# Kernel optimization log

Measured on AMD Instinct MI355X. Metric: run time of the kernel, lower is better.

Reference implementation:

```python
import jax, jax.numpy as jnp
import numpy as np

N_NODES = 50000
N_EDGES = 600000
D = 128
N_GRAPHS = 64


def setup_inputs() -> dict:
    key = jax.random.key(0)
    ks = jax.random.split(key, 16)
    x = jax.random.normal(ks[0], (N_NODES, D), dtype=jnp.float32)
    edge_index = jax.random.randint(ks[1], (2, N_EDGES), 0, N_NODES, dtype=jnp.int64)
    batch = jnp.sort(jax.random.randint(ks[2], (N_NODES,), 0, N_GRAPHS, dtype=jnp.int64))
    s = 1.0 / np.sqrt(D)
    def lin(k, out_d, in_d):
        return jax.random.uniform(k, (out_d, in_d), jnp.float32, -s, s)
    inp = {"x": x, "edge_index": edge_index, "batch": batch}
    for i, base in zip(range(3), (3, 6, 9)):
        inp[f"W_rel{i+1}"] = lin(ks[base], D, D)
        inp[f"b_rel{i+1}"] = jax.random.uniform(ks[base + 1], (D,), jnp.float32, -s, s)
        inp[f"W_root{i+1}"] = lin(ks[base + 2], D, D)
    s5 = 1.0 / np.sqrt(5)
    inp["W1"] = lin(ks[12], 5, D)
    inp["b1"] = jax.random.uniform(ks[13], (5,), jnp.float32, -s, s)
    inp["W2"] = jax.random.uniform(ks[14], (1, 5), jnp.float32, -s5, s5)
    inp["b2"] = jax.random.uniform(ks[15], (1,), jnp.float32, -s5, s5)
    return inp


def graph_conv(x, src, dst, W_rel, b_rel, W_root):
    # PyG GraphConv: out_i = W_root x_i + W_rel * sum_{j->i} x_j + b_rel
    agg = jax.ops.segment_sum(x[src], dst, num_segments=N_NODES)  # [N, D]
    return agg @ W_rel.T + b_rel + x @ W_root.T


def reference(x, edge_index, batch,
              W_rel1, b_rel1, W_root1,
              W_rel2, b_rel2, W_root2,
              W_rel3, b_rel3, W_root3,
              W1, b1, W2, b2):
    src, dst = edge_index[0], edge_index[1]
    h = jax.nn.relu(graph_conv(x, src, dst, W_rel1, b_rel1, W_root1))
    h = jax.nn.relu(graph_conv(h, src, dst, W_rel2, b_rel2, W_root2))
    h = graph_conv(h, src, dst, W_rel3, b_rel3, W_root3)
    # global max pool over graphs
    g = jax.ops.segment_max(h, batch, num_segments=N_GRAPHS)  # [G, D]
    out = jax.nn.relu(g @ W1.T + b1) @ W2.T + b2  # [G, 1]
    return out
```

## Files before the change

kernel.cpp:

```cpp
#include <hip/hip_runtime.h>
#include <float.h>

#define N_NODES 50000
#define N_EDGES 600000
#define D 128
#define N_GRAPHS 64
#define SCAN_T 256
#define SCAN_NBLK ((N_NODES + SCAN_T - 1) / SCAN_T)

typedef __attribute__((ext_vector_type(8))) short short8;
typedef __attribute__((ext_vector_type(4))) float floatx4;

__device__ inline float bf2f(unsigned short h) {
    return __uint_as_float((unsigned)h << 16);
}
__device__ inline unsigned short f2bf(float f) {
    unsigned u = __float_as_uint(f);
    return (unsigned short)((u + 0x7fffu + ((u >> 16) & 1u)) >> 16);
}


__global__ void cast_prep(const float4* __restrict__ x, ushort4* __restrict__ xb, int n4,
                          const float* __restrict__ Wr0, const float* __restrict__ Wo0,
                          const float* __restrict__ Wr1, const float* __restrict__ Wo1,
                          const float* __restrict__ Wr2, const float* __restrict__ Wo2,
                          unsigned short* __restrict__ B0, unsigned short* __restrict__ B1,
                          unsigned short* __restrict__ B2,
                          int* __restrict__ deg, float* __restrict__ g) {
    int idx = blockIdx.x * 256 + threadIdx.x;
    if (idx < N_NODES) deg[idx] = 0;
    if (idx < N_GRAPHS * D) g[idx] = -FLT_MAX;
    if (idx < n4) {
        float4 v = x[idx];
        ushort4 o;
        o.x = f2bf(v.x); o.y = f2bf(v.y); o.z = f2bf(v.z); o.w = f2bf(v.w);
        xb[idx] = o;
        return;
    }
    int w = idx - n4;
    if (w >= 3 * 128 * 256) return;
    int l = w >> 15;
    int r = w & 32767;
    int o = r >> 8, k = r & 255;
    const float* Wr = (l == 0) ? Wr0 : (l == 1) ? Wr1 : Wr2;
    const float* Wo = (l == 0) ? Wo0 : (l == 1) ? Wo1 : Wo2;
    unsigned short* B = (l == 0) ? B0 : (l == 1) ? B1 : B2;
    float v = (k < 128) ? Wr[o * 128 + k] : Wo[o * 128 + (k - 128)];
    B[r] = f2bf(v);
}


__global__ void count_deg(const int* __restrict__ ei, int* __restrict__ deg) {
    int e = blockIdx.x * 256 + threadIdx.x;
    if (e < N_EDGES) atomicAdd(&deg[ei[N_EDGES + e]], 1);
}

__global__ __launch_bounds__(SCAN_T) void block_sum(const int* __restrict__ deg,
                                                    int* __restrict__ blockSums) {
    __shared__ int s[SCAN_T];
    int tid = threadIdx.x;
    int i = blockIdx.x * SCAN_T + tid;
    s[tid] = (i < N_NODES) ? deg[i] : 0;
    __syncthreads();
    for (int off = SCAN_T / 2; off > 0; off >>= 1) {
        if (tid < off) s[tid] += s[tid + off];
        __syncthreads();
    }
    if (tid == 0) blockSums[blockIdx.x] = s[0];
}

__global__ __launch_bounds__(SCAN_T) void scan_write(const int* __restrict__ deg,
                                                     const int* __restrict__ blockSums,
                                                     int* __restrict__ row_start,
                                                     int* __restrict__ cursor) {
    __shared__ int bs[SCAN_T];
    __shared__ int s[SCAN_T];
    int tid = threadIdx.x;
    bs[tid] = (tid < SCAN_NBLK) ? blockSums[tid] : 0;
    __syncthreads();
    for (int off = 1; off < SCAN_T; off <<= 1) {
        int t = (tid >= off) ? bs[tid - off] : 0;
        __syncthreads();
        bs[tid] += t;
        __syncthreads();
    }
    int myOff = (blockIdx.x == 0) ? 0 : bs[blockIdx.x - 1];
    if (blockIdx.x == 0 && tid == SCAN_T - 1) row_start[N_NODES] = bs[tid];

    int i = blockIdx.x * SCAN_T + tid;
    int v = (i < N_NODES) ? deg[i] : 0;
    s[tid] = v;
    __syncthreads();
    for (int off = 1; off < SCAN_T; off <<= 1) {
        int t = (tid >= off) ? s[tid - off] : 0;
        __syncthreads();
        s[tid] += t;
        __syncthreads();
    }
    if (i < N_NODES) {
        int rs = myOff + s[tid] - v;
        row_start[i] = rs;
        cursor[i]    = rs;
    }
}

__global__ void fill_csr(const int* __restrict__ ei, int* __restrict__ cursor,
                         int* __restrict__ csr_src) {
    int e = blockIdx.x * 256 + threadIdx.x;
    if (e < N_EDGES) {
        int dst = ei[N_EDGES + e];
        int pos = atomicAdd(&cursor[dst], 1);
        csr_src[pos] = ei[e];
    }
}


__global__ __launch_bounds__(256) void csr_gather_bf16(
    const unsigned short* __restrict__ xb, const int* __restrict__ row_start,
    const int* __restrict__ csr_src, unsigned short* __restrict__ aggb)
{
    int node = blockIdx.x * 8 + (threadIdx.x >> 5);
    int lane = threadIdx.x & 31;
    if (node >= N_NODES) return;
    int beg = row_start[node];
    int end = row_start[node + 1];

    float a0 = 0.f, a1 = 0.f, a2 = 0.f, a3 = 0.f;
    for (int base = beg; base < end; base += 32) {
        int n = end - base; if (n > 32) n = 32;
        int idx = (lane < n) ? csr_src[base + lane] : 0;
        int j = 0;
        for (; j + 7 < n; j += 8) {
            int s0 = __shfl(idx, j,     32); int s1 = __shfl(idx, j + 1, 32);
            int s2 = __shfl(idx, j + 2, 32); int s3 = __shfl(idx, j + 3, 32);
            int s4 = __shfl(idx, j + 4, 32); int s5 = __shfl(idx, j + 5, 32);
            int s6 = __shfl(idx, j + 6, 32); int s7 = __shfl(idx, j + 7, 32);
            ushort4 u0 = *(const ushort4*)(xb + (size_t)s0 * D + lane * 4);
            ushort4 u1 = *(const ushort4*)(xb + (size_t)s1 * D + lane * 4);
            ushort4 u2 = *(const ushort4*)(xb + (size_t)s2 * D + lane * 4);
            ushort4 u3 = *(const ushort4*)(xb + (size_t)s3 * D + lane * 4);
            ushort4 u4 = *(const ushort4*)(xb + (size_t)s4 * D + lane * 4);
            ushort4 u5 = *(const ushort4*)(xb + (size_t)s5 * D + lane * 4);
            ushort4 u6 = *(const ushort4*)(xb + (size_t)s6 * D + lane * 4);
            ushort4 u7 = *(const ushort4*)(xb + (size_t)s7 * D + lane * 4);
            a0 += bf2f(u0.x) + bf2f(u1.x) + bf2f(u2.x) + bf2f(u3.x)
                + bf2f(u4.x) + bf2f(u5.x) + bf2f(u6.x) + bf2f(u7.x);
            a1 += bf2f(u0.y) + bf2f(u1.y) + bf2f(u2.y) + bf2f(u3.y)
                + bf2f(u4.y) + bf2f(u5.y) + bf2f(u6.y) + bf2f(u7.y);
            a2 += bf2f(u0.z) + bf2f(u1.z) + bf2f(u2.z) + bf2f(u3.z)
                + bf2f(u4.z) + bf2f(u5.z) + bf2f(u6.z) + bf2f(u7.z);
            a3 += bf2f(u0.w) + bf2f(u1.w) + bf2f(u2.w) + bf2f(u3.w)
                + bf2f(u4.w) + bf2f(u5.w) + bf2f(u6.w) + bf2f(u7.w);
        }
        for (; j + 3 < n; j += 4) {
            int s0 = __shfl(idx, j,     32); int s1 = __shfl(idx, j + 1, 32);
            int s2 = __shfl(idx, j + 2, 32); int s3 = __shfl(idx, j + 3, 32);
            ushort4 u0 = *(const ushort4*)(xb + (size_t)s0 * D + lane * 4);
            ushort4 u1 = *(const ushort4*)(xb + (size_t)s1 * D + lane * 4);
            ushort4 u2 = *(const ushort4*)(xb + (size_t)s2 * D + lane * 4);
            ushort4 u3 = *(const ushort4*)(xb + (size_t)s3 * D + lane * 4);
            a0 += bf2f(u0.x) + bf2f(u1.x) + bf2f(u2.x) + bf2f(u3.x);
            a1 += bf2f(u0.y) + bf2f(u1.y) + bf2f(u2.y) + bf2f(u3.y);
            a2 += bf2f(u0.z) + bf2f(u1.z) + bf2f(u2.z) + bf2f(u3.z);
            a3 += bf2f(u0.w) + bf2f(u1.w) + bf2f(u2.w) + bf2f(u3.w);
        }
        for (; j < n; ++j) {
            int s0 = __shfl(idx, j, 32);
            ushort4 u0 = *(const ushort4*)(xb + (size_t)s0 * D + lane * 4);
            a0 += bf2f(u0.x); a1 += bf2f(u0.y); a2 += bf2f(u0.z); a3 += bf2f(u0.w);
        }
    }
    ushort4 r;
    r.x = f2bf(a0); r.y = f2bf(a1); r.z = f2bf(a2); r.w = f2bf(a3);
    *(ushort4*)(aggb + (size_t)node * D + lane * 4) = r;
}


__device__ inline void stage_b_half(unsigned short* sB, const unsigned short* __restrict__ Bb,
                                    int tid, int h) {
#pragma unroll
    for (int i = 0; i < 8; ++i) {
        int flat = tid + i * 256;
        int fi = flat >> 6, ln = flat & 63;
        int mm = ln & 15, qq = ln >> 4;
        int ksL = fi >> 3, tt = fi & 7;
        short8 v = *(const short8*)(Bb + (size_t)(tt * 16 + mm) * 256
                                    + (h * 4 + ksL) * 32 + qq * 8);
        *(short8*)(sB + (size_t)flat * 8) = v;
    }
}


__global__ __launch_bounds__(256) void gemm_mfma(
    const unsigned short* __restrict__ aggb, const unsigned short* __restrict__ xb,
    const unsigned short* __restrict__ Bb, const float* __restrict__ bias,
    unsigned short* __restrict__ Ob, int relu)
{
    __shared__ unsigned short sB[16384];
    int tid  = threadIdx.x;
    int wave = tid >> 6;
    int lane = tid & 63;
    int m    = lane & 15;
    int quad = lane >> 4;
    int row0 = blockIdx.x * 64 + wave * 16;

    int arow = row0 + m;
    if (arow > N_NODES - 1) arow = N_NODES - 1;

    short8 af[8];
#pragma unroll
    for (int ks = 0; ks < 8; ++ks) {
        const unsigned short* Asrc = (ks < 4) ? aggb : xb;
        af[ks] = *(const short8*)(Asrc + (size_t)arow * 128 + (ks & 3) * 32 + quad * 8);
    }

    floatx4 acc[8];
#pragma unroll
    for (int t = 0; t < 8; ++t) acc[t] = (floatx4){0.f, 0.f, 0.f, 0.f};

    stage_b_half(sB, Bb, tid, 0);
    __syncthreads();
#pragma unroll
    for (int ksL = 0; ksL < 4; ++ksL)
#pragma unroll
        for (int t = 0; t < 8; ++t) {
            short8 b = *(const short8*)(sB + (size_t)((ksL * 8 + t) * 64 + lane) * 8);
            acc[t] = __builtin_amdgcn_mfma_f32_16x16x32_bf16(af[ksL], b, acc[t], 0, 0, 0);
        }
    __syncthreads();
    stage_b_half(sB, Bb, tid, 1);
    __syncthreads();
#pragma unroll
    for (int ksL = 0; ksL < 4; ++ksL)
#pragma unroll
        for (int t = 0; t < 8; ++t) {
            short8 b = *(const short8*)(sB + (size_t)((ksL * 8 + t) * 64 + lane) * 8);
            acc[t] = __builtin_amdgcn_mfma_f32_16x16x32_bf16(af[4 + ksL], b, acc[t], 0, 0, 0);
        }

#pragma unroll
    for (int t = 0; t < 8; ++t) {
        int col = t * 16 + m;
        float bv = bias[col];
#pragma unroll
        for (int r = 0; r < 4; ++r) {
            int row = row0 + quad * 4 + r;
            if (row >= N_NODES) continue;
            float v = acc[t][r] + bv;
            if (relu) v = fmaxf(v, 0.f);
            Ob[(size_t)row * D + col] = f2bf(v);
        }
    }
}


struct PoolShared {
    union {
        unsigned short b[16384];
        float c[64 * 129];
    };
};

__global__ __launch_bounds__(256) void gemm_pool(
    const unsigned short* __restrict__ aggb, const unsigned short* __restrict__ xb,
    const unsigned short* __restrict__ Bb, const float* __restrict__ bias,
    const int* __restrict__ batch, float* __restrict__ g)
{
    __shared__ PoolShared sh;
    __shared__ int bl[64];
    int tid  = threadIdx.x;
    int wave = tid >> 6;
    int lane = tid & 63;
    int m    = lane & 15;
    int quad = lane >> 4;
    int row0 = blockIdx.x * 64;

    int arow = row0 + wave * 16 + m;
    if (arow > N_NODES - 1) arow = N_NODES - 1;

    short8 af[8];
#pragma unroll
    for (int ks = 0; ks < 8; ++ks) {
        const unsigned short* Asrc = (ks < 4) ? aggb : xb;
        af[ks] = *(const short8*)(Asrc + (size_t)arow * 128 + (ks & 3) * 32 + quad * 8);
    }

    floatx4 acc[8];
#pragma unroll
    for (int t = 0; t < 8; ++t) acc[t] = (floatx4){0.f, 0.f, 0.f, 0.f};

    stage_b_half(sh.b, Bb, tid, 0);
    __syncthreads();
#pragma unroll
    for (int ksL = 0; ksL < 4; ++ksL)
#pragma unroll
        for (int t = 0; t < 8; ++t) {
            short8 b = *(const short8*)(sh.b + (size_t)((ksL * 8 + t) * 64 + lane) * 8);
            acc[t] = __builtin_amdgcn_mfma_f32_16x16x32_bf16(af[ksL], b, acc[t], 0, 0, 0);
        }
    __syncthreads();
    stage_b_half(sh.b, Bb, tid, 1);
    __syncthreads();
#pragma unroll
    for (int ksL = 0; ksL < 4; ++ksL)
#pragma unroll
        for (int t = 0; t < 8; ++t) {
            short8 b = *(const short8*)(sh.b + (size_t)((ksL * 8 + t) * 64 + lane) * 8);
            acc[t] = __builtin_amdgcn_mfma_f32_16x16x32_bf16(af[4 + ksL], b, acc[t], 0, 0, 0);
        }
    __syncthreads();

#pragma unroll
    for (int t = 0; t < 8; ++t) {
        int col = t * 16 + m;
        float bv = bias[col];
#pragma unroll
        for (int r = 0; r < 4; ++r)
            sh.c[(wave * 16 + quad * 4 + r) * 129 + col] = acc[t][r] + bv;
    }
    if (tid < 64) {
        int grow = row0 + tid;
        bl[tid] = (grow < N_NODES) ? batch[grow] : -1;
    }
    __syncthreads();

    int nvalid = min(64, N_NODES - row0);
    int b0 = bl[0], b1 = bl[nvalid - 1];
    int col  = tid & 127;
    int rbeg = (tid >> 7) * 32;
    for (int gg = b0; gg <= b1; ++gg) {
        float cur = -FLT_MAX;
#pragma unroll
        for (int r = 0; r < 32; ++r) {
            int rr = rbeg + r;
            float v = (bl[rr] == gg) ? sh.c[rr * 129 + col] : -FLT_MAX;
            cur = fmaxf(cur, v);
        }
        if (cur > -FLT_MAX) {
            float* ad = &g[gg * D + col];
            if (cur >= 0.f) atomicMax((int*)ad, __float_as_int(cur));
            else            atomicMin((unsigned int*)ad, __float_as_uint(cur));
        }
    }
}


__global__ void mlp_head(const float* __restrict__ g,
                         const float* __restrict__ W1, const float* __restrict__ b1,
                         const float* __restrict__ W2, const float* __restrict__ b2,
                         float* __restrict__ out) {
    int gi = threadIdx.x;
    if (gi >= N_GRAPHS) return;
    float h[5];
#pragma unroll
    for (int j = 0; j < 5; ++j) {
        float acc = b1[j];
        for (int k = 0; k < D; ++k) acc += g[gi * D + k] * W1[j * D + k];
        h[j] = fmaxf(acc, 0.f);
    }
    float o = b2[0];
#pragma unroll
    for (int j = 0; j < 5; ++j) o += h[j] * W2[j];
    out[gi] = o;
}

extern "C" void kernel_launch(void* const* d_in, const int* in_sizes, int n_in,
                              void* d_out, int out_size, void* d_ws, size_t ws_size,
                              hipStream_t stream) {
    const float* x     = (const float*)d_in[0];
    const int*   ei    = (const int*)d_in[1];
    const int*   batch = (const int*)d_in[2];
    const float* Wrel[3]  = {(const float*)d_in[3], (const float*)d_in[6], (const float*)d_in[9]};
    const float* brel[3]  = {(const float*)d_in[4], (const float*)d_in[7], (const float*)d_in[10]};
    const float* Wroot[3] = {(const float*)d_in[5], (const float*)d_in[8], (const float*)d_in[11]};
    const float* W1 = (const float*)d_in[12];
    const float* b1 = (const float*)d_in[13];
    const float* W2 = (const float*)d_in[14];
    const float* b2 = (const float*)d_in[15];
    float* out = (float*)d_out;

    char* ws = (char*)d_ws;
    const size_t nodeB16 = (size_t)N_NODES * D * sizeof(unsigned short);
    unsigned short* xb   = (unsigned short*)(ws);
    unsigned short* aggb = (unsigned short*)(ws + nodeB16);
    unsigned short* hb1  = (unsigned short*)(ws + 2 * nodeB16);
    unsigned short* hb2  = (unsigned short*)(ws + 3 * nodeB16);
    char* p = ws + 4 * nodeB16;
    unsigned short* Bb0 = (unsigned short*)p;   p += 128 * 256 * sizeof(unsigned short);
    unsigned short* Bb1 = (unsigned short*)p;   p += 128 * 256 * sizeof(unsigned short);
    unsigned short* Bb2 = (unsigned short*)p;   p += 128 * 256 * sizeof(unsigned short);
    float* g        = (float*)p;                p += N_GRAPHS * D * sizeof(float);
    int*   deg      = (int*)p;                  p += N_NODES * sizeof(int);
    int*   row_start= (int*)p;                  p += (N_NODES + 1) * sizeof(int);
    int*   cursor   = (int*)p;                  p += N_NODES * sizeof(int);
    int*   csr_src  = (int*)p;                  p += N_EDGES * sizeof(int);
    int*   blockSums= (int*)p;                  p += SCAN_NBLK * sizeof(int);

    const int n4 = N_NODES * D / 4;
    const int cast_total = n4 + 3 * 128 * 256;
    cast_prep<<<(cast_total + 255) / 256, 256, 0, stream>>>(
        (const float4*)x, (ushort4*)xb, n4,
        Wrel[0], Wroot[0], Wrel[1], Wroot[1], Wrel[2], Wroot[2],
        Bb0, Bb1, Bb2, deg, g);

    count_deg<<<(N_EDGES + 255) / 256, 256, 0, stream>>>(ei, deg);
    block_sum<<<SCAN_NBLK, SCAN_T, 0, stream>>>(deg, blockSums);
    scan_write<<<SCAN_NBLK, SCAN_T, 0, stream>>>(deg, blockSums, row_start, cursor);
    fill_csr<<<(N_EDGES + 255) / 256, 256, 0, stream>>>(ei, cursor, csr_src);

    const int ggrid = (N_NODES + 7) / 8;
    const int mgrid = (N_NODES + 63) / 64;

    csr_gather_bf16<<<ggrid, 256, 0, stream>>>(xb, row_start, csr_src, aggb);
    gemm_mfma<<<mgrid, 256, 0, stream>>>(aggb, xb, Bb0, brel[0], hb1, 1);

    csr_gather_bf16<<<ggrid, 256, 0, stream>>>(hb1, row_start, csr_src, aggb);
    gemm_mfma<<<mgrid, 256, 0, stream>>>(aggb, hb1, Bb1, brel[1], hb2, 1);

    csr_gather_bf16<<<ggrid, 256, 0, stream>>>(hb2, row_start, csr_src, aggb);
    gemm_pool<<<mgrid, 256, 0, stream>>>(aggb, hb2, Bb2, brel[2], batch, g);

    mlp_head<<<1, 64, 0, stream>>>(g, W1, b1, W2, b2, out);
}
```

Measured before the change: 309.8 us.

## Fuse CSR neighbor gather into MFMA GEMM kernels via swizzled LDS tile

After: 327.2 us. 5.6% more time.

```diff
diff --git a/kernel.cpp b/kernel.cpp
--- a/kernel.cpp
+++ b/kernel.cpp
@@ -115,64 +115,70 @@
 }
 
 
-__global__ __launch_bounds__(256) void csr_gather_bf16(
-    const unsigned short* __restrict__ xb, const int* __restrict__ row_start,
-    const int* __restrict__ csr_src, unsigned short* __restrict__ aggb)
+#define ACC8(u) { a[0] += bf2f((unsigned short)(u)[0]); a[1] += bf2f((unsigned short)(u)[1]); \
+                  a[2] += bf2f((unsigned short)(u)[2]); a[3] += bf2f((unsigned short)(u)[3]); \
+                  a[4] += bf2f((unsigned short)(u)[4]); a[5] += bf2f((unsigned short)(u)[5]); \
+                  a[6] += bf2f((unsigned short)(u)[6]); a[7] += bf2f((unsigned short)(u)[7]); }
+
+__device__ inline void gather_tile(const unsigned short* __restrict__ xb,
+                                   const int* __restrict__ row_start,
+                                   const int* __restrict__ csr_src,
+                                   unsigned short* sA, int row0, int tid)
 {
-    int node = blockIdx.x * 8 + (threadIdx.x >> 5);
-    int lane = threadIdx.x & 31;
-    if (node >= N_NODES) return;
-    int beg = row_start[node];
-    int end = row_start[node + 1];
-
-    float a0 = 0.f, a1 = 0.f, a2 = 0.f, a3 = 0.f;
-    for (int base = beg; base < end; base += 32) {
-        int n = end - base; if (n > 32) n = 32;
-        int idx = (lane < n) ? csr_src[base + lane] : 0;
-        int j = 0;
-        for (; j + 7 < n; j += 8) {
-            int s0 = __shfl(idx, j,     32); int s1 = __shfl(idx, j + 1, 32);
-            int s2 = __shfl(idx, j + 2, 32); int s3 = __shfl(idx, j + 3, 32);
-            int s4 = __shfl(idx, j + 4, 32); int s5 = __shfl(idx, j + 5, 32);
-            int s6 = __shfl(idx, j + 6, 32); int s7 = __shfl(idx, j + 7, 32);
-            ushort4 u0 = *(const ushort4*)(xb + (size_t)s0 * D + lane * 4);
-            ushort4 u1 = *(const ushort4*)(xb + (size_t)s1 * D + lane * 4);
-            ushort4 u2 = *(const ushort4*)(xb + (size_t)s2 * D + lane * 4);
-            ushort4 u3 = *(const ushort4*)(xb + (size_t)s3 * D + lane * 4);
-            ushort4 u4 = *(const ushort4*)(xb + (size_t)s4 * D + lane * 4);
-            ushort4 u5 = *(const ushort4*)(xb + (size_t)s5 * D + lane * 4);
-            ushort4 u6 = *(const ushort4*)(xb + (size_t)s6 * D + lane * 4);
-            ushort4 u7 = *(const ushort4*)(xb + (size_t)s7 * D + lane * 4);
-            a0 += bf2f(u0.x) + bf2f(u1.x) + bf2f(u2.x) + bf2f(u3.x)
-                + bf2f(u4.x) + bf2f(u5.x) + bf2f(u6.x) + bf2f(u7.x);
-            a1 += bf2f(u0.y) + bf2f(u1.y) + bf2f(u2.y) + bf2f(u3.y)
-                + bf2f(u4.y) + bf2f(u5.y) + bf2f(u6.y) + bf2f(u7.y);
-            a2 += bf2f(u0.z) + bf2f(u1.z) + bf2f(u2.z) + bf2f(u3.z)
-                + bf2f(u4.z) + bf2f(u5.z) + bf2f(u6.z) + bf2f(u7.z);
-            a3 += bf2f(u0.w) + bf2f(u1.w) + bf2f(u2.w) + bf2f(u3.w)
-                + bf2f(u4.w) + bf2f(u5.w) + bf2f(u6.w) + bf2f(u7.w);
-        }
-        for (; j + 3 < n; j += 4) {
-            int s0 = __shfl(idx, j,     32); int s1 = __shfl(idx, j + 1, 32);
-            int s2 = __shfl(idx, j + 2, 32); int s3 = __shfl(idx, j + 3, 32);
-            ushort4 u0 = *(const ushort4*)(xb + (size_t)s0 * D + lane * 4);
-            ushort4 u1 = *(const ushort4*)(xb + (size_t)s1 * D + lane * 4);
-            ushort4 u2 = *(const ushort4*)(xb + (size_t)s2 * D + lane * 4);
-            ushort4 u3 = *(const ushort4*)(xb + (size_t)s3 * D + lane * 4);
-            a0 += bf2f(u0.x) + bf2f(u1.x) + bf2f(u2.x) + bf2f(u3.x);
-            a1 += bf2f(u0.y) + bf2f(u1.y) + bf2f(u2.y) + bf2f(u3.y);
-            a2 += bf2f(u0.z) + bf2f(u1.z) + bf2f(u2.z) + bf2f(u3.z);
-            a3 += bf2f(u0.w) + bf2f(u1.w) + bf2f(u2.w) + bf2f(u3.w);
-        }
-        for (; j < n; ++j) {
-            int s0 = __shfl(idx, j, 32);
-            ushort4 u0 = *(const ushort4*)(xb + (size_t)s0 * D + lane * 4);
-            a0 += bf2f(u0.x); a1 += bf2f(u0.y); a2 += bf2f(u0.z); a3 += bf2f(u0.w);
-        }
-    }
-    ushort4 r;
-    r.x = f2bf(a0); r.y = f2bf(a1); r.z = f2bf(a2); r.w = f2bf(a3);
-    *(ushort4*)(aggb + (size_t)node * D + lane * 4) = r;
+    int grp = tid >> 4;
+    int ln  = tid & 15;
+#pragma unroll 1
+    for (int pass = 0; pass < 4; ++pass) {
+        int r = pass * 16 + grp;
+        int node = row0 + r;
+        float a[8];
+#pragma unroll
+        for (int i = 0; i < 8; ++i) a[i] = 0.f;
+        if (node < N_NODES) {
+            int beg = row_start[node];
+            int end = row_start[node + 1];
+            for (int base = beg; base < end; base += 16) {
+                int n = end - base; if (n > 16) n = 16;
+                int idx = (ln < n) ? csr_src[base + ln] : 0;
+                int j = 0;
+                for (; j + 7 < n; j += 8) {
+                    int s0 = __shfl(idx, j,     16); int s1 = __shfl(idx, j + 1, 16);
+                    int s2 = __shfl(idx, j + 2, 16); int s3 = __shfl(idx, j + 3, 16);
+                    int s4 = __shfl(idx, j + 4, 16); int s5 = __shfl(idx, j + 5, 16);
+                    int s6 = __shfl(idx, j + 6, 16); int s7 = __shfl(idx, j + 7, 16);
+                    short8 u0 = *(const short8*)(xb + (size_t)s0 * D + ln * 8);
+                    short8 u1 = *(const short8*)(xb + (size_t)s1 * D + ln * 8);
+                    short8 u2 = *(const short8*)(xb + (size_t)s2 * D + ln * 8);
+                    short8 u3 = *(const short8*)(xb + (size_t)s3 * D + ln * 8);
+                    short8 u4 = *(const short8*)(xb + (size_t)s4 * D + ln * 8);
+                    short8 u5 = *(const short8*)(xb + (size_t)s5 * D + ln * 8);
+                    short8 u6 = *(const short8*)(xb + (size_t)s6 * D + ln * 8);
+                    short8 u7 = *(const short8*)(xb + (size_t)s7 * D + ln * 8);
+                    ACC8(u0); ACC8(u1); ACC8(u2); ACC8(u3);
+                    ACC8(u4); ACC8(u5); ACC8(u6); ACC8(u7);
+                }
+                for (; j + 3 < n; j += 4) {
+                    int s0 = __shfl(idx, j,     16); int s1 = __shfl(idx, j + 1, 16);
+                    int s2 = __shfl(idx, j + 2, 16); int s3 = __shfl(idx, j + 3, 16);
+                    short8 u0 = *(const short8*)(xb + (size_t)s0 * D + ln * 8);
+                    short8 u1 = *(const short8*)(xb + (size_t)s1 * D + ln * 8);
+                    short8 u2 = *(const short8*)(xb + (size_t)s2 * D + ln * 8);
+                    short8 u3 = *(const short8*)(xb + (size_t)s3 * D + ln * 8);
+                    ACC8(u0); ACC8(u1); ACC8(u2); ACC8(u3);
+                }
+                for (; j < n; ++j) {
+                    int s0 = __shfl(idx, j, 16);
+                    short8 u0 = *(const short8*)(xb + (size_t)s0 * D + ln * 8);
+                    ACC8(u0);
+                }
+            }
+        }
+        short8 v;
+#pragma unroll
+        for (int i = 0; i < 8; ++i) v[i] = (short)f2bf(a[i]);
+        int slot = r * 16 + (ln ^ (r & 7));
+        *(short8*)((char*)sA + (size_t)slot * 16) = v;
+    }
 }
 
 
@@ -191,41 +197,53 @@
 }
 
 
-__global__ __launch_bounds__(256) void gemm_mfma(
-    const unsigned short* __restrict__ aggb, const unsigned short* __restrict__ xb,
-    const unsigned short* __restrict__ Bb, const float* __restrict__ bias,
-    unsigned short* __restrict__ Ob, int relu)
+__global__ __launch_bounds__(256) void layer_fused(
+    const unsigned short* __restrict__ xb, const int* __restrict__ row_start,
+    const int* __restrict__ csr_src, const unsigned short* __restrict__ Bb,
+    const float* __restrict__ bias, unsigned short* __restrict__ Ob, int relu)
 {
+    __shared__ unsigned short sA[64 * 128];
     __shared__ unsigned short sB[16384];
     int tid  = threadIdx.x;
+    int row0 = blockIdx.x * 64;
+
+    gather_tile(xb, row_start, csr_src, sA, row0, tid);
+
     int wave = tid >> 6;
     int lane = tid & 63;
     int m    = lane & 15;
     int quad = lane >> 4;
-    int row0 = blockIdx.x * 64 + wave * 16;
-
-    int arow = row0 + m;
+
+    int arow = row0 + wave * 16 + m;
     if (arow > N_NODES - 1) arow = N_NODES - 1;
-
-    short8 af[8];
-#pragma unroll
-    for (int ks = 0; ks < 8; ++ks) {
-        const unsigned short* Asrc = (ks < 4) ? aggb : xb;
-        af[ks] = *(const short8*)(Asrc + (size_t)arow * 128 + (ks & 3) * 32 + quad * 8);
+    short8 afX[4];
+#pragma unroll
+    for (int ks = 0; ks < 4; ++ks)
+        afX[ks] = *(const short8*)(xb + (size_t)arow * 128 + ks * 32 + quad * 8);
+
+    stage_b_half(sB, Bb, tid, 0);
+    __syncthreads();
+
+    short8 afA[4];
+    {
+        int r = wave * 16 + m;
+#pragma unroll
+        for (int ksL = 0; ksL < 4; ++ksL) {
+            int slot = r * 16 + ((ksL * 4 + quad) ^ (r & 7));
+            afA[ksL] = *(const short8*)((const char*)sA + (size_t)slot * 16);
+        }
     }
 
     floatx4 acc[8];
 #pragma unroll
     for (int t = 0; t < 8; ++t) acc[t] = (floatx4){0.f, 0.f, 0.f, 0.f};
 
-    stage_b_half(sB, Bb, tid, 0);
-    __syncthreads();
 #pragma unroll
     for (int ksL = 0; ksL < 4; ++ksL)
 #pragma unroll
         for (int t = 0; t < 8; ++t) {
             short8 b = *(const short8*)(sB + (size_t)((ksL * 8 + t) * 64 + lane) * 8);
-            acc[t] = __builtin_amdgcn_mfma_f32_16x16x32_bf16(af[ksL], b, acc[t], 0, 0, 0);
+            acc[t] = __builtin_amdgcn_mfma_f32_16x16x32_bf16(afA[ksL], b, acc[t], 0, 0, 0);
         }
     __syncthreads();
     stage_b_half(sB, Bb, tid, 1);
@@ -235,7 +253,7 @@
 #pragma unroll
         for (int t = 0; t < 8; ++t) {
             short8 b = *(const short8*)(sB + (size_t)((ksL * 8 + t) * 64 + lane) * 8);
-            acc[t] = __builtin_amdgcn_mfma_f32_16x16x32_bf16(af[4 + ksL], b, acc[t], 0, 0, 0);
+            acc[t] = __builtin_amdgcn_mfma_f32_16x16x32_bf16(afX[ksL], b, acc[t], 0, 0, 0);
         }
 
 #pragma unroll
@@ -244,7 +262,7 @@
         float bv = bias[col];
 #pragma unroll
         for (int r = 0; r < 4; ++r) {
-            int row = row0 + quad * 4 + r;
+            int row = row0 + wave * 16 + quad * 4 + r;
             if (row >= N_NODES) continue;
             float v = acc[t][r] + bv;
             if (relu) v = fmaxf(v, 0.f);
@@ -261,42 +279,58 @@
     };
 };
 
-__global__ __launch_bounds__(256) void gemm_pool(
-    const unsigned short* __restrict__ aggb, const unsigned short* __restrict__ xb,
-    const unsigned short* __restrict__ Bb, const float* __restrict__ bias,
-    const int* __restrict__ batch, float* __restrict__ g)
+__global__ __launch_bounds__(256) void layer_pool(
+    const unsigned short* __restrict__ xb, const int* __restrict__ row_start,
+    const int* __restrict__ csr_src, const unsigned short* __restrict__ Bb,
+    const float* __restrict__ bias, const int* __restrict__ batch, float* __restrict__ g)
 {
+    __shared__ unsigned short sA[64 * 128];
     __shared__ PoolShared sh;
     __shared__ int bl[64];
     int tid  = threadIdx.x;
+    int row0 = blockIdx.x * 64;
+
+    gather_tile(xb, row_start, csr_src, sA, row0, tid);
+
     int wave = tid >> 6;
     int lane = tid & 63;
     int m    = lane & 15;
     int quad = lane >> 4;
-    int row0 = blockIdx.x * 64;
 
     int arow = row0 + wave * 16 + m;
     if (arow > N_NODES - 1) arow = N_NODES - 1;
-
-    short8 af[8];
-#pragma unroll
-    for (int ks = 0; ks < 8; ++ks) {
-        const unsigned short* Asrc = (ks < 4) ? aggb : xb;
-        af[ks] = *(const short8*)(Asrc + (size_t)arow * 128 + (ks & 3) * 32 + quad * 8);
+    short8 afX[4];
+#pragma unroll
+    for (int ks = 0; ks < 4; ++ks)
+        afX[ks] = *(const short8*)(xb + (size_t)arow * 128 + ks * 32 + quad * 8);
+
+    if (tid < 64) {
+        int grow = row0 + tid;
+        bl[tid] = (grow < N_NODES) ? batch[grow] : -1;
+    }
+    stage_b_half(sh.b, Bb, tid, 0);
+    __syncthreads();
+
+    short8 afA[4];
+    {
+        int r = wave * 16 + m;
+#pragma unroll
+        for (int ksL = 0; ksL < 4; ++ksL) {
+            int slot = r * 16 + ((ksL * 4 + quad) ^ (r & 7));
+            afA[ksL] = *(const short8*)((const char*)sA + (size_t)slot * 16);
+        }
     }
 
     floatx4 acc[8];
 #pragma unroll
     for (int t = 0; t < 8; ++t) acc[t] = (floatx4){0.f, 0.f, 0.f, 0.f};
 
-    stage_b_half(sh.b, Bb, tid, 0);
-    __syncthreads();
 #pragma unroll
     for (int ksL = 0; ksL < 4; ++ksL)
 #pragma unroll
         for (int t = 0; t < 8; ++t) {
             short8 b = *(const short8*)(sh.b + (size_t)((ksL * 8 + t) * 64 + lane) * 8);
-            acc[t] = __builtin_amdgcn_mfma_f32_16x16x32_bf16(af[ksL], b, acc[t], 0, 0, 0);
+            acc[t] = __builtin_amdgcn_mfma_f32_16x16x32_bf16(afA[ksL], b, acc[t], 0, 0, 0);
         }
     __syncthreads();
     stage_b_half(sh.b, Bb, tid, 1);
@@ -306,7 +340,7 @@
 #pragma unroll
         for (int t = 0; t < 8; ++t) {
             short8 b = *(const short8*)(sh.b + (size_t)((ksL * 8 + t) * 64 + lane) * 8);
-            acc[t] = __builtin_amdgcn_mfma_f32_16x16x32_bf16(af[4 + ksL], b, acc[t], 0, 0, 0);
+            acc[t] = __builtin_amdgcn_mfma_f32_16x16x32_bf16(afX[ksL], b, acc[t], 0, 0, 0);
         }
     __syncthreads();
 
@@ -317,10 +351,6 @@
 #pragma unroll
         for (int r = 0; r < 4; ++r)
             sh.c[(wave * 16 + quad * 4 + r) * 129 + col] = acc[t][r] + bv;
-    }
-    if (tid < 64) {
-        int grow = row0 + tid;
-        bl[tid] = (grow < N_NODES) ? batch[grow] : -1;
     }
     __syncthreads();
 
@@ -345,23 +375,23 @@
 }
 
 
-__global__ void mlp_head(const float* __restrict__ g,
+__global__ __launch_bounds__(64) void mlp_head(const float* __restrict__ g,
                          const float* __restrict__ W1, const float* __restrict__ b1,
                          const float* __restrict__ W2, const float* __restrict__ b2,
                          float* __restrict__ out) {
-    int gi = threadIdx.x;
-    if (gi >= N_GRAPHS) return;
-    float h[5];
+    int gi = blockIdx.x;
+    int lane = threadIdx.x;
+    float x0 = g[gi * D + lane];
+    float x1 = g[gi * D + 64 + lane];
+    float o = b2[0];
 #pragma unroll
     for (int j = 0; j < 5; ++j) {
-        float acc = b1[j];
-        for (int k = 0; k < D; ++k) acc += g[gi * D + k] * W1[j * D + k];
-        h[j] = fmaxf(acc, 0.f);
-    }
-    float o = b2[0];
-#pragma unroll
-    for (int j = 0; j < 5; ++j) o += h[j] * W2[j];
-    out[gi] = o;
+        float p = x0 * W1[j * D + lane] + x1 * W1[j * D + 64 + lane];
+#pragma unroll
+        for (int off = 32; off > 0; off >>= 1) p += __shfl_xor(p, off, 64);
+        o += fmaxf(p + b1[j], 0.f) * W2[j];
+    }
+    if (lane == 0) out[gi] = o;
 }
 
 extern "C" void kernel_launch(void* const* d_in, const int* in_sizes, int n_in,
@@ -382,10 +412,9 @@
     char* ws = (char*)d_ws;
     const size_t nodeB16 = (size_t)N_NODES * D * sizeof(unsigned short);
     unsigned short* xb   = (unsigned short*)(ws);
-    unsigned short* aggb = (unsigned short*)(ws + nodeB16);
-    unsigned short* hb1  = (unsigned short*)(ws + 2 * nodeB16);
-    unsigned short* hb2  = (unsigned short*)(ws + 3 * nodeB16);
-    char* p = ws + 4 * nodeB16;
+    unsigned short* hb1  = (unsigned short*)(ws + nodeB16);
+    unsigned short* hb2  = (unsigned short*)(ws + 2 * nodeB16);
+    char* p = ws + 3 * nodeB16;
     unsigned short* Bb0 = (unsigned short*)p;   p += 128 * 256 * sizeof(unsigned short);
     unsigned short* Bb1 = (unsigned short*)p;   p += 128 * 256 * sizeof(unsigned short);
     unsigned short* Bb2 = (unsigned short*)p;   p += 128 * 256 * sizeof(unsigned short);
@@ -408,17 +437,11 @@
     scan_write<<<SCAN_NBLK, SCAN_T, 0, stream>>>(deg, blockSums, row_start, cursor);
     fill_csr<<<(N_EDGES + 255) / 256, 256, 0, stream>>>(ei, cursor, csr_src);
 
-    const int ggrid = (N_NODES + 7) / 8;
     const int mgrid = (N_NODES + 63) / 64;
 
-    csr_gather_bf16<<<ggrid, 256, 0, stream>>>(xb, row_start, csr_src, aggb);
-    gemm_mfma<<<mgrid, 256, 0, stream>>>(aggb, xb, Bb0, brel[0], hb1, 1);
-
-    csr_gather_bf16<<<ggrid, 256, 0, stream>>>(hb1, row_start, csr_src, aggb);
-    gemm_mfma<<<mgrid, 256, 0, stream>>>(aggb, hb1, Bb1, brel[1], hb2, 1);
-
-    csr_gather_bf16<<<ggrid, 256, 0, stream>>>(hb2, row_start, csr_src, aggb);
-    gemm_pool<<<mgrid, 256, 0, stream>>>(aggb, hb2, Bb2, brel[2], batch, g);
-
-    mlp_head<<<1, 64, 0, stream>>>(g, W1, b1, W2, b2, out);
-}
+    layer_fused<<<mgrid, 256, 0, stream>>>(xb,  row_start, csr_src, Bb0, brel[0], hb1, 1);
+    layer_fused<<<mgrid, 256, 0, stream>>>(hb1, row_start, csr_src, Bb1, brel[1], hb2, 1);
+    layer_pool <<<mgrid, 256, 0, stream>>>(hb2, row_start, csr_src, Bb2, brel[2], batch, g);
+
+    mlp_head<<<N_GRAPHS, 64, 0, stream>>>(g, W1, b1, W2, b2, out);
+}
```

## Split node features into two 64-column halves and gather each half separately

Applied to the files above, without the earlier changes.

Measured after the change: 321.8 us. 3.9% more time.

```diff
diff --git a/kernel.cpp b/kernel.cpp
--- a/kernel.cpp
+++ b/kernel.cpp
@@ -20,7 +20,8 @@
 }
 
 
-__global__ void cast_prep(const float4* __restrict__ x, ushort4* __restrict__ xb, int n4,
+__global__ void cast_prep(const float4* __restrict__ x,
+                          ushort4* __restrict__ xb0, ushort4* __restrict__ xb1, int n4,
                           const float* __restrict__ Wr0, const float* __restrict__ Wo0,
                           const float* __restrict__ Wr1, const float* __restrict__ Wo1,
                           const float* __restrict__ Wr2, const float* __restrict__ Wo2,
@@ -34,7 +35,10 @@
         float4 v = x[idx];
         ushort4 o;
         o.x = f2bf(v.x); o.y = f2bf(v.y); o.z = f2bf(v.z); o.w = f2bf(v.w);
-        xb[idx] = o;
+        int node = idx >> 5;
+        int q    = idx & 31;
+        ushort4* dst = (q < 16) ? xb0 : xb1;
+        dst[(size_t)node * 16 + (q & 15)] = o;
         return;
     }
     int w = idx - n4;
@@ -115,64 +119,66 @@
 }
 
 
-__global__ __launch_bounds__(256) void csr_gather_bf16(
-    const unsigned short* __restrict__ xb, const int* __restrict__ row_start,
-    const int* __restrict__ csr_src, unsigned short* __restrict__ aggb)
+#define ACC8(u) { a[0] += bf2f((unsigned short)(u)[0]); a[1] += bf2f((unsigned short)(u)[1]); \
+                  a[2] += bf2f((unsigned short)(u)[2]); a[3] += bf2f((unsigned short)(u)[3]); \
+                  a[4] += bf2f((unsigned short)(u)[4]); a[5] += bf2f((unsigned short)(u)[5]); \
+                  a[6] += bf2f((unsigned short)(u)[6]); a[7] += bf2f((unsigned short)(u)[7]); }
+
+__global__ __launch_bounds__(256) void gather_half(
+    const unsigned short* __restrict__ xh,
+    const int* __restrict__ row_start, const int* __restrict__ csr_src,
+    unsigned short* __restrict__ aggh)
 {
-    int node = blockIdx.x * 8 + (threadIdx.x >> 5);
-    int lane = threadIdx.x & 31;
+    int grp  = threadIdx.x >> 3;
+    int ln   = threadIdx.x & 7;
+    int node = blockIdx.x * 32 + grp;
     if (node >= N_NODES) return;
     int beg = row_start[node];
     int end = row_start[node + 1];
 
-    float a0 = 0.f, a1 = 0.f, a2 = 0.f, a3 = 0.f;
-    for (int base = beg; base < end; base += 32) {
-        int n = end - base; if (n > 32) n = 32;
-        int idx = (lane < n) ? csr_src[base + lane] : 0;
+    float a[8];
+#pragma unroll
+    for (int i = 0; i < 8; ++i) a[i] = 0.f;
+
+    for (int base = beg; base < end; base += 8) {
+        int n = end - base; if (n > 8) n = 8;
+        int idx = (ln < n) ? csr_src[base + ln] : 0;
         int j = 0;
         for (; j + 7 < n; j += 8) {
-            int s0 = __shfl(idx, j,     32); int s1 = __shfl(idx, j + 1, 32);
-            int s2 = __shfl(idx, j + 2, 32); int s3 = __shfl(idx, j + 3, 32);
-            int s4 = __shfl(idx, j + 4, 32); int s5 = __shfl(idx, j + 5, 32);
-            int s6 = __shfl(idx, j + 6, 32); int s7 = __shfl(idx, j + 7, 32);
-            ushort4 u0 = *(const ushort4*)(xb + (size_t)s0 * D + lane * 4);
-            ushort4 u1 = *(const ushort4*)(xb + (size_t)s1 * D + lane * 4);
-            ushort4 u2 = *(const ushort4*)(xb + (size_t)s2 * D + lane * 4);
-            ushort4 u3 = *(const ushort4*)(xb + (size_t)s3 * D + lane * 4);
-            ushort4 u4 = *(const ushort4*)(xb + (size_t)s4 * D + lane * 4);
-            ushort4 u5 = *(const ushort4*)(xb + (size_t)s5 * D + lane * 4);
-            ushort4 u6 = *(const ushort4*)(xb + (size_t)s6 * D + lane * 4);
-            ushort4 u7 = *(const ushort4*)(xb + (size_t)s7 * D + lane * 4);
-            a0 += bf2f(u0.x) + bf2f(u1.x) + bf2f(u2.x) + bf2f(u3.x)
-                + bf2f(u4.x) + bf2f(u5.x) + bf2f(u6.x) + bf2f(u7.x);
-            a1 += bf2f(u0.y) + bf2f(u1.y) + bf2f(u2.y) + bf2f(u3.y)
-                + bf2f(u4.y) + bf2f(u5.y) + bf2f(u6.y) + bf2f(u7.y);
-            a2 += bf2f(u0.z) + bf2f(u1.z) + bf2f(u2.z) + bf2f(u3.z)
-                + bf2f(u4.z) + bf2f(u5.z) + bf2f(u6.z) + bf2f(u7.z);
-            a3 += bf2f(u0.w) + bf2f(u1.w) + bf2f(u2.w) + bf2f(u3.w)
-                + bf2f(u4.w) + bf2f(u5.w) + bf2f(u6.w) + bf2f(u7.w);
+            int s0 = __shfl(idx, 0, 8); int s1 = __shfl(idx, 1, 8);
+            int s2 = __shfl(idx, 2, 8); int s3 = __shfl(idx, 3, 8);
+            int s4 = __shfl(idx, 4, 8); int s5 = __shfl(idx, 5, 8);
+            int s6 = __shfl(idx, 6, 8); int s7 = __shfl(idx, 7, 8);
+            short8 u0 = *(const short8*)(xh + (size_t)s0 * 64 + ln * 8);
+            short8 u1 = *(const short8*)(xh + (size_t)s1 * 64 + ln * 8);
+            short8 u2 = *(const short8*)(xh + (size_t)s2 * 64 + ln * 8);
+            short8 u3 = *(const short8*)(xh + (size_t)s3 * 64 + ln * 8);
+            short8 u4 = *(const short8*)(xh + (size_t)s4 * 64 + ln * 8);
+            short8 u5 = *(const short8*)(xh + (size_t)s5 * 64 + ln * 8);
+            short8 u6 = *(const short8*)(xh + (size_t)s6 * 64 + ln * 8);
+            short8 u7 = *(const short8*)(xh + (size_t)s7 * 64 + ln * 8);
+            ACC8(u0); ACC8(u1); ACC8(u2); ACC8(u3);
+            ACC8(u4); ACC8(u5); ACC8(u6); ACC8(u7);
         }
         for (; j + 3 < n; j += 4) {
-            int s0 = __shfl(idx, j,     32); int s1 = __shfl(idx, j + 1, 32);
-            int s2 = __shfl(idx, j + 2, 32); int s3 = __shfl(idx, j + 3, 32);
-            ushort4 u0 = *(const ushort4*)(xb + (size_t)s0 * D + lane * 4);
-            ushort4 u1 = *(const ushort4*)(xb + (size_t)s1 * D + lane * 4);
-            ushort4 u2 = *(const ushort4*)(xb + (size_t)s2 * D + lane * 4);
-            ushort4 u3 = *(const ushort4*)(xb + (size_t)s3 * D + lane * 4);
-            a0 += bf2f(u0.x) + bf2f(u1.x) + bf2f(u2.x) + bf2f(u3.x);
-            a1 += bf2f(u0.y) + bf2f(u1.y) + bf2f(u2.y) + bf2f(u3.y);
-            a2 += bf2f(u0.z) + bf2f(u1.z) + bf2f(u2.z) + bf2f(u3.z);
-            a3 += bf2f(u0.w) + bf2f(u1.w) + bf2f(u2.w) + bf2f(u3.w);
+            int s0 = __shfl(idx, j,     8); int s1 = __shfl(idx, j + 1, 8);
+            int s2 = __shfl(idx, j + 2, 8); int s3 = __shfl(idx, j + 3, 8);
+            short8 u0 = *(const short8*)(xh + (size_t)s0 * 64 + ln * 8);
+            short8 u1 = *(const short8*)(xh + (size_t)s1 * 64 + ln * 8);
+            short8 u2 = *(const short8*)(xh + (size_t)s2 * 64 + ln * 8);
+            short8 u3 = *(const short8*)(xh + (size_t)s3 * 64 + ln * 8);
+            ACC8(u0); ACC8(u1); ACC8(u2); ACC8(u3);
         }
         for (; j < n; ++j) {
-            int s0 = __shfl(idx, j, 32);
-            ushort4 u0 = *(const ushort4*)(xb + (size_t)s0 * D + lane * 4);
-            a0 += bf2f(u0.x); a1 += bf2f(u0.y); a2 += bf2f(u0.z); a3 += bf2f(u0.w);
-        }
-    }
-    ushort4 r;
-    r.x = f2bf(a0); r.y = f2bf(a1); r.z = f2bf(a2); r.w = f2bf(a3);
-    *(ushort4*)(aggb + (size_t)node * D + lane * 4) = r;
+            int s0 = __shfl(idx, j, 8);
+            short8 u0 = *(const short8*)(xh + (size_t)s0 * 64 + ln * 8);
+            ACC8(u0);
+        }
+    }
+    short8 r;
+#pragma unroll
+    for (int i = 0; i < 8; ++i) r[i] = (short)f2bf(a[i]);
+    *(short8*)(aggh + (size_t)node * 64 + ln * 8) = r;
 }
 
 
@@ -192,9 +198,10 @@
 
 
 __global__ __launch_bounds__(256) void gemm_mfma(
-    const unsigned short* __restrict__ aggb, const unsigned short* __restrict__ xb,
+    const unsigned short* __restrict__ agg0, const unsigned short* __restrict__ agg1,
+    const unsigned short* __restrict__ x0,   const unsigned short* __restrict__ x1,
     const unsigned short* __restrict__ Bb, const float* __restrict__ bias,
-    unsigned short* __restrict__ Ob, int relu)
+    unsigned short* __restrict__ O0, unsigned short* __restrict__ O1, int relu)
 {
     __shared__ unsigned short sB[16384];
     int tid  = threadIdx.x;
@@ -210,8 +217,9 @@
     short8 af[8];
 #pragma unroll
     for (int ks = 0; ks < 8; ++ks) {
-        const unsigned short* Asrc = (ks < 4) ? aggb : xb;
-        af[ks] = *(const short8*)(Asrc + (size_t)arow * 128 + (ks & 3) * 32 + quad * 8);
+        const unsigned short* Asrc =
+            (ks < 2) ? agg0 : (ks < 4) ? agg1 : (ks < 6) ? x0 : x1;
+        af[ks] = *(const short8*)(Asrc + (size_t)arow * 64 + (ks & 1) * 32 + quad * 8);
     }
 
     floatx4 acc[8];
@@ -242,13 +250,14 @@
     for (int t = 0; t < 8; ++t) {
         int col = t * 16 + m;
         float bv = bias[col];
+        unsigned short* Oh = (t < 4) ? O0 : O1;
 #pragma unroll
         for (int r = 0; r < 4; ++r) {
             int row = row0 + quad * 4 + r;
             if (row >= N_NODES) continue;
             float v = acc[t][r] + bv;
             if (relu) v = fmaxf(v, 0.f);
-            Ob[(size_t)row * D + col] = f2bf(v);
+            Oh[(size_t)row * 64 + (col & 63)] = f2bf(v);
         }
     }
 }
@@ -262,7 +271,8 @@
 };
 
 __global__ __launch_bounds__(256) void gemm_pool(
-    const unsigned short* __restrict__ aggb, const unsigned short* __restrict__ xb,
+    const unsigned short* __restrict__ agg0, const unsigned short* __restrict__ agg1,
+    const unsigned short* __restrict__ x0,   const unsigned short* __restrict__ x1,
     const unsigned short* __restrict__ Bb, const float* __restrict__ bias,
     const int* __restrict__ batch, float* __restrict__ g)
 {
@@ -281,14 +291,19 @@
     short8 af[8];
 #pragma unroll
     for (int ks = 0; ks < 8; ++ks) {
-        const unsigned short* Asrc = (ks < 4) ? aggb : xb;
-        af[ks] = *(const short8*)(Asrc + (size_t)arow * 128 + (ks & 3) * 32 + quad * 8);
+        const unsigned short* Asrc =
+            (ks < 2) ? agg0 : (ks < 4) ? agg1 : (ks < 6) ? x0 : x1;
+        af[ks] = *(const short8*)(Asrc + (size_t)arow * 64 + (ks & 1) * 32 + quad * 8);
     }
 
     floatx4 acc[8];
 #pragma unroll
     for (int t = 0; t < 8; ++t) acc[t] = (floatx4){0.f, 0.f, 0.f, 0.f};
 
+    if (tid < 64) {
+        int grow = row0 + tid;
+        bl[tid] = (grow < N_NODES) ? batch[grow] : -1;
+    }
     stage_b_half(sh.b, Bb, tid, 0);
     __syncthreads();
 #pragma unroll
@@ -317,10 +332,6 @@
 #pragma unroll
         for (int r = 0; r < 4; ++r)
             sh.c[(wave * 16 + quad * 4 + r) * 129 + col] = acc[t][r] + bv;
-    }
-    if (tid < 64) {
-        int grow = row0 + tid;
-        bl[tid] = (grow < N_NODES) ? batch[grow] : -1;
     }
     __syncthreads();
 
@@ -345,23 +356,23 @@
 }
 
 
-__global__ void mlp_head(const float* __restrict__ g,
+__global__ __launch_bounds__(64) void mlp_head(const float* __restrict__ g,
                          const float* __restrict__ W1, const float* __restrict__ b1,
                          const float* __restrict__ W2, const float* __restrict__ b2,
                          float* __restrict__ out) {
-    int gi = threadIdx.x;
-    if (gi >= N_GRAPHS) return;
-    float h[5];
+    int gi = blockIdx.x;
+    int lane = threadIdx.x;
+    float x0 = g[gi * D + lane];
+    float x1 = g[gi * D + 64 + lane];
+    float o = b2[0];
 #pragma unroll
     for (int j = 0; j < 5; ++j) {
-        float acc = b1[j];
-        for (int k = 0; k < D; ++k) acc += g[gi * D + k] * W1[j * D + k];
-        h[j] = fmaxf(acc, 0.f);
-    }
-    float o = b2[0];
-#pragma unroll
-    for (int j = 0; j < 5; ++j) o += h[j] * W2[j];
-    out[gi] = o;
+        float p = x0 * W1[j * D + lane] + x1 * W1[j * D + 64 + lane];
+#pragma unroll
+        for (int off = 32; off > 0; off >>= 1) p += __shfl_xor(p, off, 64);
+        o += fmaxf(p + b1[j], 0.f) * W2[j];
+    }
+    if (lane == 0) out[gi] = o;
 }
 
 extern "C" void kernel_launch(void* const* d_in, const int* in_sizes, int n_in,
@@ -380,12 +391,16 @@
     float* out = (float*)d_out;
 
     char* ws = (char*)d_ws;
-    const size_t nodeB16 = (size_t)N_NODES * D * sizeof(unsigned short);
-    unsigned short* xb   = (unsigned short*)(ws);
-    unsigned short* aggb = (unsigned short*)(ws + nodeB16);
-    unsigned short* hb1  = (unsigned short*)(ws + 2 * nodeB16);
-    unsigned short* hb2  = (unsigned short*)(ws + 3 * nodeB16);
-    char* p = ws + 4 * nodeB16;
+    const size_t halfB = (size_t)N_NODES * 64 * sizeof(unsigned short);
+    unsigned short* xb0  = (unsigned short*)(ws);
+    unsigned short* xb1  = (unsigned short*)(ws + 1 * halfB);
+    unsigned short* hb10 = (unsigned short*)(ws + 2 * halfB);
+    unsigned short* hb11 = (unsigned short*)(ws + 3 * halfB);
+    unsigned short* hb20 = (unsigned short*)(ws + 4 * halfB);
+    unsigned short* hb21 = (unsigned short*)(ws + 5 * halfB);
+    unsigned short* ag0  = (unsigned short*)(ws + 6 * halfB);
+    unsigned short* ag1  = (unsigned short*)(ws + 7 * halfB);
+    char* p = ws + 8 * halfB;
     unsigned short* Bb0 = (unsigned short*)p;   p += 128 * 256 * sizeof(unsigned short);
     unsigned short* Bb1 = (unsigned short*)p;   p += 128 * 256 * sizeof(unsigned short);
     unsigned short* Bb2 = (unsigned short*)p;   p += 128 * 256 * sizeof(unsigned short);
@@ -399,7 +414,7 @@
     const int n4 = N_NODES * D / 4;
     const int cast_total = n4 + 3 * 128 * 256;
     cast_prep<<<(cast_total + 255) / 256, 256, 0, stream>>>(
-        (const float4*)x, (ushort4*)xb, n4,
+        (const float4*)x, (ushort4*)xb0, (ushort4*)xb1, n4,
         Wrel[0], Wroot[0], Wrel[1], Wroot[1], Wrel[2], Wroot[2],
         Bb0, Bb1, Bb2, deg, g);
 
@@ -408,17 +423,18 @@
     scan_write<<<SCAN_NBLK, SCAN_T, 0, stream>>>(deg, blockSums, row_start, cursor);
     fill_csr<<<(N_EDGES + 255) / 256, 256, 0, stream>>>(ei, cursor, csr_src);
 
-    const int ggrid = (N_NODES + 7) / 8;
+    const int ggrid = (N_NODES + 31) / 32;
     const int mgrid = (N_NODES + 63) / 64;
 
-    csr_gather_bf16<<<ggrid, 256, 0, stream>>>(xb, row_start, csr_src, aggb);
-    gemm_mfma<<<mgrid, 256, 0, stream>>>(aggb, xb, Bb0, brel[0], hb1, 1);
-
-    csr_gather_bf16<<<ggrid, 256, 0, stream>>>(hb1, row_start, csr_src, aggb);
-    gemm_mfma<<<mgrid, 256, 0, stream>>>(aggb, hb1, Bb1, brel[1], hb2, 1);
-
-    csr_gather_bf16<<<ggrid, 256, 0, stream>>>(hb2, row_start, csr_src, aggb);
-    gemm_pool<<<mgrid, 256, 0, stream>>>(aggb, hb2, Bb2, brel[2], batch, g);
-
-    mlp_head<<<1, 64, 0, stream>>>(g, W1, b1, W2, b2, out);
-}
+    gather_half<<<ggrid, 256, 0, stream>>>(xb0, row_start, csr_src, ag0);
+    gather_half<<<ggrid, 256, 0, stream>>>(xb1, row_start, csr_src, ag1);
+    gemm_mfma<<<mgrid, 256, 0, stream>>>(ag0, ag1, xb0, xb1, Bb0, brel[0], hb10, hb11, 1);
+    gather_half<<<ggrid, 256, 0, stream>>>(hb10, row_start, csr_src, ag0);
+    gather_half<<<ggrid, 256, 0, stream>>>(hb11, row_start, csr_src, ag1);
+    gemm_mfma<<<mgrid, 256, 0, stream>>>(ag0, ag1, hb10, hb11, Bb1, brel[1], hb20, hb21, 1);
+    gather_half<<<ggrid, 256, 0, stream>>>(hb20, row_start, csr_src, ag0);
+    gather_half<<<ggrid, 256, 0, stream>>>(hb21, row_start, csr_src, ag1);
+    gemm_pool<<<mgrid, 256, 0, stream>>>(ag0, ag1, hb20, hb21, Bb2, brel[2], batch, g);
+
+    mlp_head<<<N_GRAPHS, 64, 0, stream>>>(g, W1, b1, W2, b2, out);
+}
```
